# Kernel tuning notes

Measured on AMD Instinct MI355X. Metric: run time of the kernel, lower is better.

Reference implementation:

```python
import jax, jax.numpy as jnp
import numpy as np

N = 200000          # num nodes (num_rus)
E = 12800000        # num edges (avg degree 64)
IN_C, HID, OUT = 1, 16, 4


def setup_inputs() -> dict:
    key = jax.random.key(0)
    ks = jax.random.split(key, 6)
    x = jax.random.normal(ks[0], (N, IN_C), dtype=jnp.float32)
    edges = jax.random.randint(ks[1], (2, E), 0, N, dtype=jnp.int64)
    W1 = jax.random.normal(ks[2], (IN_C, HID), dtype=jnp.float32) / np.sqrt(IN_C)
    b1 = jnp.zeros((HID,), dtype=jnp.float32)
    W2 = jax.random.normal(ks[3], (HID, HID), dtype=jnp.float32) / np.sqrt(HID)
    b2 = jnp.zeros((HID,), dtype=jnp.float32)
    Wl = jax.random.normal(ks[4], (HID, OUT), dtype=jnp.float32) / np.sqrt(HID)
    bl = jnp.zeros((OUT,), dtype=jnp.float32)
    return {"x": x, "edges": edges, "W1": W1, "b1": b1, "W2": W2, "b2": b2, "Wl": Wl, "bl": bl}


def _gcn_norm(edges):
    # PyG GCNConv default: add self-loops, symmetric normalization.
    loops = jnp.arange(N, dtype=edges.dtype)
    src = jnp.concatenate([edges[0], loops])   # [E+N]
    dst = jnp.concatenate([edges[1], loops])
    deg = jax.ops.segment_sum(jnp.ones_like(dst, dtype=jnp.float32), dst, num_segments=N)
    dinv = jnp.where(deg > 0, jax.lax.rsqrt(deg), 0.0)
    norm = dinv[src] * dinv[dst]               # [E+N]
    return src, dst, norm


def _gcn_conv(h, W, b, src, dst, norm):
    m = h @ W                                  # [N, out] transform first (cheap, small C)
    msgs = m[src] * norm[:, None]              # gather + normalize, [E+N, out]
    agg = jax.ops.segment_sum(msgs, dst, num_segments=N)
    return agg + b


def reference(x, edges, W1, b1, W2, b2, Wl, bl):
    src, dst, norm = _gcn_norm(edges)
    h = jax.nn.relu(_gcn_conv(x, W1, b1, src, dst, norm))
    h = jax.nn.relu(_gcn_conv(h, W2, b2, src, dst, norm))
    return h @ Wl + bl                         # [N, 4]
```

## Files before the change

kernel.cpp:

```cpp
#include <hip/hip_runtime.h>

#define HID 16
#define OUTC 4
#define G 64
#define SBSH 8
#define SBN 256
#define CAP 21504
#define PHSH 16
#define SUBK 8
#define KB (SBN * SUBK)
#define PBLK 512
#define NPB_MAX 800
#define NPB_H 400
#define STCAP 46
#define STP 47
#define EPB 16
#define EPP (PBLK * EPB)
#define SENT 0xFFFFFFFFu

__device__ __forceinline__ float relu(float v) { return v > 0.f ? v : 0.f; }

__global__ void k_cnt(const int* __restrict__ dst, int* __restrict__ cnt,
                      int E, int nsb, int nc, int ncsh) {
    __shared__ int lc[NPB_MAX];
    for (int i = threadIdx.x; i < nsb; i += PBLK) lc[i] = 0;
    __syncthreads();
    int c = blockIdx.x;
    int chunk = (E + nc - 1) / nc;
    int lo = c * chunk, hi = lo + chunk < E ? lo + chunk : E;
    for (int i = lo + threadIdx.x; i < hi; i += PBLK * 4) {
#pragma unroll
        for (int u = 0; u < 4; ++u) {
            int ii = i + u * PBLK;
            if (ii < hi) atomicAdd(lc + (dst[ii] >> SBSH), 1);
        }
    }
    __syncthreads();
    for (int b = threadIdx.x; b < nsb; b += PBLK)
        cnt[(b << ncsh) + c] = (lc[b] + 15) & ~15;
}

__global__ void k_scanA(int* __restrict__ a, int* __restrict__ bsum, int L) {
    __shared__ int s[1024];
    int i = blockIdx.x * 1024 + threadIdx.x;
    int v = (i < L) ? a[i] : 0;
    s[threadIdx.x] = v; __syncthreads();
    for (int off = 1; off < 1024; off <<= 1) {
        int t = (threadIdx.x >= (unsigned)off) ? s[threadIdx.x - off] : 0;
        __syncthreads();
        s[threadIdx.x] += t;
        __syncthreads();
    }
    if (i < L) a[i] = s[threadIdx.x] - v;
    if (threadIdx.x == 1023) bsum[blockIdx.x] = s[1023];
}

__global__ void k_scanB(int* __restrict__ bsum, int SB) {
    __shared__ int s[1024];
    int carry = 0;
    for (int base = 0; base < SB; base += 1024) {
        int idx = base + threadIdx.x;
        int v = (idx < SB) ? bsum[idx] : 0;
        s[threadIdx.x] = v; __syncthreads();
        for (int off = 1; off < 1024; off <<= 1) {
            int t = (threadIdx.x >= (unsigned)off) ? s[threadIdx.x - off] : 0;
            __syncthreads();
            s[threadIdx.x] += t;
            __syncthreads();
        }
        if (idx < SB) bsum[idx] = carry + s[threadIdx.x] - v;
        carry += s[1023];
        __syncthreads();
    }
    if (threadIdx.x == 0) bsum[SB] = carry;
}

__global__ void k_scanC(int* __restrict__ a, const int* __restrict__ bsum,
                        int* __restrict__ bOff, int L, int nsb, int SB,
                        int nc, int ncsh) {
    int i = blockIdx.x * 1024 + threadIdx.x;
    if (i < L) {
        int v = a[i] + bsum[blockIdx.x];
        a[i] = v;
        if ((i & (nc - 1)) == 0) bOff[i >> ncsh] = v;
    }
    if (blockIdx.x == 0 && threadIdx.x == 0) bOff[nsb] = bsum[SB];
}

__global__ void __launch_bounds__(PBLK) k_part(const int* __restrict__ src,
                                               const int* __restrict__ dst,
                                               const int* __restrict__ cnt,
                                               unsigned int* __restrict__ rec,
                                               int E, int nsb, int nc, int ncsh) {
    __shared__ unsigned int stage[NPB_H * STP];
    __shared__ int scnt[NPB_H];
    __shared__ int gcur[NPB_H];
    int c = blockIdx.x >> 1, h = blockIdx.x & 1;
    int nh = (nsb - h + 1) >> 1;
    for (int bh = threadIdx.x; bh < nh; bh += PBLK) {
        scnt[bh] = 0;
        gcur[bh] = cnt[((bh * 2 + h) << ncsh) + c];
    }
    __syncthreads();
    int chunk = (E + nc - 1) / nc;
    int lo = c * chunk, hi = lo + chunk < E ? lo + chunk : E;
    int g4 = threadIdx.x >> 2, r4 = threadIdx.x & 3;
    for (int base = lo; base < hi; base += EPP) {
#pragma unroll 4
        for (int k = 0; k < EPB; ++k) {
            int i = base + k * PBLK + threadIdx.x;
            if (i < hi) {
                int d = dst[i], s = src[i];
                int b = d >> SBSH;
                if ((b & 1) == h) {
                    int bh = b >> 1;
                    int pos = atomicAdd(scnt + bh, 1);
                    if (pos < STCAP)
                        stage[bh * STP + pos] = (unsigned int)s | ((unsigned int)(d & (SBN - 1)) << 18);
                }
            }
        }
        __syncthreads();
        for (int bh = g4; bh < nh; bh += PBLK / 4) {
            int n = scnt[bh];
            int f = n & ~15;
            if (f > 0) {
                int gc = gcur[bh];
                for (int j = 0; j < f; j += 16) {
                    const unsigned int* sp = &stage[bh * STP + j] + r4 * 4;
                    ((uint4*)&rec[gc + j])[r4] = make_uint4(sp[0], sp[1], sp[2], sp[3]);
                }
                if (r4 == 0) {
                    gcur[bh] = gc + f;
                    for (int jj = 0; jj < n - f; ++jj)
                        stage[bh * STP + jj] = stage[bh * STP + f + jj];
                    scnt[bh] = n - f;
                }
            }
        }
        __syncthreads();
    }
    for (int bh = threadIdx.x; bh < nh; bh += PBLK) {
        int n = scnt[bh];
        if (n > 0) {
            unsigned int tmp[16];
            for (int j = 0; j < 16; ++j) tmp[j] = (j < n) ? stage[bh * STP + j] : SENT;
            uint4* d4 = (uint4*)&rec[gcur[bh]];
            d4[0] = make_uint4(tmp[0], tmp[1], tmp[2], tmp[3]);
            d4[1] = make_uint4(tmp[4], tmp[5], tmp[6], tmp[7]);
            d4[2] = make_uint4(tmp[8], tmp[9], tmp[10], tmp[11]);
            d4[3] = make_uint4(tmp[12], tmp[13], tmp[14], tmp[15]);
        }
    }
}

__global__ void __launch_bounds__(256) k_sort(const int* __restrict__ bOff,
                                              unsigned int* __restrict__ rec,
                                              float* __restrict__ dinv,
                                              int* __restrict__ rowp,
                                              int N, int nsb, int E) {
    __shared__ unsigned int raw[CAP];
    __shared__ int hist[KB], cur[KB];
    __shared__ int s[256];
    int b = blockIdx.x;
    int beg = bOff[b], end = bOff[b + 1];
    int size = end - beg; if (size > CAP) size = CAP;
    {
        uint4* raw4 = (uint4*)raw;
        const uint4* rec4 = (const uint4*)&rec[beg];
        int size4 = size >> 2;
        for (int i = threadIdx.x; i < size4; i += 256) raw4[i] = rec4[i];
    }
    for (int k = threadIdx.x; k < KB; k += 256) hist[k] = 0;
    __syncthreads();
    for (int i = threadIdx.x; i < size; i += 1024) {
#pragma unroll
        for (int u = 0; u < 4; ++u) {
            int ii = i + u * 256;
            if (ii < size) {
                unsigned int r = raw[ii];
                if (r != SENT) {
                    int key = (int)((r >> 18) << 3) | (int)((r & 0x3FFFF) >> PHSH);
                    atomicAdd(hist + key, 1);
                }
            }
        }
    }
    __syncthreads();
    int t = threadIdx.x;
    int psum = 0;
#pragma unroll
    for (int j = 0; j < SUBK; ++j) psum += hist[t * SUBK + j];
    s[t] = psum; __syncthreads();
    for (int off = 1; off < 256; off <<= 1) {
        int v = (t >= off) ? s[t - off] : 0;
        __syncthreads();
        s[t] += v;
        __syncthreads();
    }
    int ex = s[t] - psum;
    {
        int n = b * SBN + t;
        bool valid = (n < N);
        int running = ex;
#pragma unroll
        for (int j = 0; j < SUBK; ++j) {
            cur[t * SUBK + j] = running;
            if (valid) rowp[(size_t)n * SUBK + j] = beg + running;
            running += hist[t * SUBK + j];
        }
        if (valid) dinv[n] = rsqrtf((float)psum + 1.0f);
    }
    __syncthreads();
    for (int i = t; i < size; i += 1024) {
#pragma unroll
        for (int u = 0; u < 4; ++u) {
            int ii = i + u * 256;
            if (ii < size) {
                unsigned int r = raw[ii];
                if (r != SENT) {
                    int key = (int)((r >> 18) << 3) | (int)((r & 0x3FFFF) >> PHSH);
                    int p = atomicAdd(cur + key, 1);
                    rec[beg + p] = r & 0x3FFFF;
                }
            }
        }
    }
}

__global__ void k_m1(const float* __restrict__ x, const float* __restrict__ W1,
                     const float* __restrict__ dinv, float* __restrict__ m, int N) {
    int t = blockIdx.x * blockDim.x + threadIdx.x;
    if (t < N * HID) {
        int n = t >> 4, c = t & 15;
        m[t] = x[n] * W1[c] * dinv[n];
    }
}

__global__ void k_m2(float4* __restrict__ h4, const float* __restrict__ W2,
                     const float* __restrict__ dinv, int N) {
    __shared__ float hs[64][HID + 1];
    __shared__ float w[HID * HID];
    if (threadIdx.x < HID * HID) w[threadIdx.x] = W2[threadIdx.x];
    int idx = blockIdx.x * 256 + threadIdx.x;
    int n = idx >> 2, q = idx & 3;
    int ln = threadIdx.x >> 2;
    if (n < N) {
        float4 v = h4[idx];
        hs[ln][q * 4 + 0] = v.x; hs[ln][q * 4 + 1] = v.y;
        hs[ln][q * 4 + 2] = v.z; hs[ln][q * 4 + 3] = v.w;
    }
    __syncthreads();
    if (n < N) {
        float dn = dinv[n];
        float4 acc = make_float4(0.f, 0.f, 0.f, 0.f);
        const float* hr = hs[ln];
#pragma unroll
        for (int ci = 0; ci < HID; ++ci) {
            float hv = hr[ci];
            const float* wr = w + ci * HID + q * 4;
            acc.x += hv * wr[0]; acc.y += hv * wr[1];
            acc.z += hv * wr[2]; acc.w += hv * wr[3];
        }
        acc.x *= dn; acc.y *= dn; acc.z *= dn; acc.w *= dn;
        h4[idx] = acc;
    }
}

template <int MODE>
__global__ void __launch_bounds__(256) k_aggp(const int* __restrict__ rowp,
                                              const unsigned int* __restrict__ adj,
                                              const float* __restrict__ dinv,
                                              const float4* __restrict__ mS4,
                                              float4* __restrict__ gagg4,
                                              const float4* __restrict__ b4,
                                              const float* __restrict__ Wl,
                                              const float* __restrict__ bl,
                                              float* __restrict__ out,
                                              int N, int p) {
    __shared__ float hs[G][HID + 1];
    __shared__ float wl[HID * OUTC];
    __shared__ float blv[OUTC];
    if (MODE == 2) {
        if (threadIdx.x < HID * OUTC) wl[threadIdx.x] = Wl[threadIdx.x];
        if (threadIdx.x < OUTC) blv[threadIdx.x] = bl[threadIdx.x];
    }
    int dl = threadIdx.x >> 2, q = threadIdx.x & 3;
    int n = blockIdx.x * G + dl;
    if (n < N) {
        int i = rowp[(size_t)n * SUBK + p];
        int end = rowp[(size_t)n * SUBK + p + 1];
        float4 acc = (p == 0) ? mS4[n * 4 + q] : gagg4[n * 4 + q];
        for (; i + 8 <= end; i += 8) {
            int s0 = adj[i] * 4 + q, s1 = adj[i + 1] * 4 + q;
            int s2 = adj[i + 2] * 4 + q, s3 = adj[i + 3] * 4 + q;
            int s4 = adj[i + 4] * 4 + q, s5 = adj[i + 5] * 4 + q;
            int s6 = adj[i + 6] * 4 + q, s7 = adj[i + 7] * 4 + q;
            float4 v0 = mS4[s0], v1 = mS4[s1], v2 = mS4[s2], v3 = mS4[s3];
            float4 v4 = mS4[s4], v5 = mS4[s5], v6 = mS4[s6], v7 = mS4[s7];
            acc.x += (v0.x + v1.x + v2.x + v3.x) + (v4.x + v5.x + v6.x + v7.x);
            acc.y += (v0.y + v1.y + v2.y + v3.y) + (v4.y + v5.y + v6.y + v7.y);
            acc.z += (v0.z + v1.z + v2.z + v3.z) + (v4.z + v5.z + v6.z + v7.z);
            acc.w += (v0.w + v1.w + v2.w + v3.w) + (v4.w + v5.w + v6.w + v7.w);
        }
        for (; i + 4 <= end; i += 4) {
            int s0 = adj[i] * 4 + q, s1 = adj[i + 1] * 4 + q;
            int s2 = adj[i + 2] * 4 + q, s3 = adj[i + 3] * 4 + q;
            float4 v0 = mS4[s0], v1 = mS4[s1], v2 = mS4[s2], v3 = mS4[s3];
            acc.x += v0.x + v1.x + v2.x + v3.x;
            acc.y += v0.y + v1.y + v2.y + v3.y;
            acc.z += v0.z + v1.z + v2.z + v3.z;
            acc.w += v0.w + v1.w + v2.w + v3.w;
        }
        for (; i < end; ++i) {
            float4 v = mS4[adj[i] * 4 + q];
            acc.x += v.x; acc.y += v.y; acc.z += v.z; acc.w += v.w;
        }
        if (MODE == 0) {
            gagg4[n * 4 + q] = acc;
        } else {
            float dn = dinv[n];
            float4 bb = b4[q];
            float4 h;
            h.x = relu(acc.x * dn + bb.x);
            h.y = relu(acc.y * dn + bb.y);
            h.z = relu(acc.z * dn + bb.z);
            h.w = relu(acc.w * dn + bb.w);
            if (MODE == 1) {
                gagg4[n * 4 + q] = h;
            } else {
                hs[dl][q * 4 + 0] = h.x; hs[dl][q * 4 + 1] = h.y;
                hs[dl][q * 4 + 2] = h.z; hs[dl][q * 4 + 3] = h.w;
            }
        }
    }
    if (MODE == 2) {
        __syncthreads();
        if (n < N) {
            float acc = blv[q];
            const float* hr = hs[dl];
#pragma unroll
            for (int ci = 0; ci < HID; ++ci) acc += hr[ci] * wl[ci * OUTC + q];
            out[n * OUTC + q] = acc;
        }
    }
}

static inline size_t alignup(size_t v, size_t a) { return (v + a - 1) & ~(a - 1); }

extern "C" void kernel_launch(void* const* d_in, const int* in_sizes, int n_in,
                              void* d_out, int out_size, void* d_ws, size_t ws_size,
                              hipStream_t stream) {
    const float* x  = (const float*)d_in[0];
    const int* ed   = (const int*)d_in[1];
    const float* W1 = (const float*)d_in[2];
    const float* b1 = (const float*)d_in[3];
    const float* W2 = (const float*)d_in[4];
    const float* b2 = (const float*)d_in[5];
    const float* Wl = (const float*)d_in[6];
    const float* bl = (const float*)d_in[7];
    float* out      = (float*)d_out;

    int N = in_sizes[0];
    int E = in_sizes[1] / 2;
    const int* src = ed;
    const int* dst = ed + E;
    int nsb = (N + SBN - 1) / SBN;
    int nb64 = (N + G - 1) / G;
    int nphase = (N + (1 << PHSH) - 1) >> PHSH;

    int nc = 256, ncsh = 8;
    size_t o = 0;
    float* dinv; int* rowp; int* bsum; int* bOff; unsigned int* rec;
    float* bufA; float* bufB;
    char* w = (char*)d_ws;
    for (int attempt = 0; attempt < 2; ++attempt) {
        int L = nsb * nc;
        int SB = (L + 1023) / 1024;
        size_t Epad = (size_t)E + 15 * (size_t)L;
        o = 0;
        dinv = (float*)(w + o); o = alignup(o + (size_t)N * 4, 64);
        rowp = (int*)(w + o);   o = alignup(o + (size_t)N * SUBK * 4, 64);
        bsum = (int*)(w + o);   o = alignup(o + ((size_t)SB + 1) * 4, 64);
        bOff = (int*)(w + o);   o = alignup(o + ((size_t)nsb + 1) * 4, 64);
        rec  = (unsigned int*)(w + o); o = alignup(o + Epad * 4, 64);
        bufA = (float*)(w + o); o = alignup(o + (size_t)N * HID * 4, 64);
        bufB = (float*)(w + o); o = alignup(o + (size_t)N * HID * 4, 64);
        if (o <= ws_size || nc == 128) break;
        nc = 128; ncsh = 7;
    }
    int L = nsb * nc;
    int SB = (L + 1023) / 1024;
    int* cnt = (int*)bufA;

    int blk = 256;
    int gN16 = (N * HID + blk - 1) / blk;

    k_cnt<<<nc, PBLK, 0, stream>>>(dst, cnt, E, nsb, nc, ncsh);
    k_scanA<<<SB, 1024, 0, stream>>>(cnt, bsum, L);
    k_scanB<<<1, 1024, 0, stream>>>(bsum, SB);
    k_scanC<<<SB, 1024, 0, stream>>>(cnt, bsum, bOff, L, nsb, SB, nc, ncsh);
    k_part<<<nc * 2, PBLK, 0, stream>>>(src, dst, cnt, rec, E, nsb, nc, ncsh);
    k_sort<<<nsb, 256, 0, stream>>>(bOff, rec, dinv, rowp, N, nsb, E);

    k_m1<<<gN16, blk, 0, stream>>>(x, W1, dinv, bufA, N);
    for (int p = 0; p < nphase; ++p) {
        if (p < nphase - 1)
            k_aggp<0><<<nb64, blk, 0, stream>>>(rowp, rec, dinv, (const float4*)bufA,
                                                (float4*)bufB, (const float4*)b1,
                                                nullptr, nullptr, nullptr, N, p);
        else
            k_aggp<1><<<nb64, blk, 0, stream>>>(rowp, rec, dinv, (const float4*)bufA,
                                                (float4*)bufB, (const float4*)b1,
                                                nullptr, nullptr, nullptr, N, p);
    }

    k_m2<<<nb64, blk, 0, stream>>>((float4*)bufB, W2, dinv, N);
    for (int p = 0; p < nphase; ++p) {
        if (p < nphase - 1)
            k_aggp<0><<<nb64, blk, 0, stream>>>(rowp, rec, dinv, (const float4*)bufB,
                                                (float4*)bufA, (const float4*)b2,
                                                nullptr, nullptr, nullptr, N, p);
        else
            k_aggp<2><<<nb64, blk, 0, stream>>>(rowp, rec, dinv, (const float4*)bufB,
                                                (float4*)bufA, (const float4*)b2,
                                                Wl, bl, out, N, p);
    }
}
```

Baseline: 538.2 us.

## Partition all superbuckets in one k_part block per chunk instead of two halves

k_part used to launch two blocks per edge chunk, each staging only the even or the odd superbuckets, so every edge's src/dst was read twice. Now one block per chunk stages all superbuckets in a single larger shared-memory buffer (784 buckets × 45 slots), so edge input is read only once. In exchange each block needs far more LDS (about 147KB), which likely limits each CU to one resident block. There are also half as many blocks and a slightly smaller per-bucket staging capacity, which reduces parallelism and latency hiding in this pass.

```diff
diff --git a/kernel.cpp b/kernel.cpp
--- a/kernel.cpp
+++ b/kernel.cpp
@@ -10,10 +10,9 @@
 #define SUBK 8
 #define KB (SBN * SUBK)
 #define PBLK 512
-#define NPB_MAX 800
-#define NPB_H 400
-#define STCAP 46
-#define STP 47
+#define NPB_MAX 784
+#define STCAP 45
+#define STP 45
 #define EPB 16
 #define EPP (PBLK * EPB)
 #define SENT 0xFFFFFFFFu
@@ -92,14 +91,13 @@
                                                const int* __restrict__ cnt,
                                                unsigned int* __restrict__ rec,
                                                int E, int nsb, int nc, int ncsh) {
-    __shared__ unsigned int stage[NPB_H * STP];
-    __shared__ int scnt[NPB_H];
-    __shared__ int gcur[NPB_H];
-    int c = blockIdx.x >> 1, h = blockIdx.x & 1;
-    int nh = (nsb - h + 1) >> 1;
-    for (int bh = threadIdx.x; bh < nh; bh += PBLK) {
-        scnt[bh] = 0;
-        gcur[bh] = cnt[((bh * 2 + h) << ncsh) + c];
+    __shared__ unsigned int stage[NPB_MAX * STP];
+    __shared__ int scnt[NPB_MAX];
+    __shared__ int gcur[NPB_MAX];
+    int c = blockIdx.x;
+    for (int b = threadIdx.x; b < nsb; b += PBLK) {
+        scnt[b] = 0;
+        gcur[b] = cnt[(b << ncsh) + c];
     }
     __syncthreads();
     int chunk = (E + nc - 1) / nc;
@@ -112,40 +110,37 @@
             if (i < hi) {
                 int d = dst[i], s = src[i];
                 int b = d >> SBSH;
-                if ((b & 1) == h) {
-                    int bh = b >> 1;
-                    int pos = atomicAdd(scnt + bh, 1);
-                    if (pos < STCAP)
-                        stage[bh * STP + pos] = (unsigned int)s | ((unsigned int)(d & (SBN - 1)) << 18);
-                }
+                int pos = atomicAdd(scnt + b, 1);
+                if (pos < STCAP)
+                    stage[b * STP + pos] = (unsigned int)s | ((unsigned int)(d & (SBN - 1)) << 18);
             }
         }
         __syncthreads();
-        for (int bh = g4; bh < nh; bh += PBLK / 4) {
-            int n = scnt[bh];
+        for (int b = g4; b < nsb; b += PBLK / 4) {
+            int n = scnt[b];
             int f = n & ~15;
             if (f > 0) {
-                int gc = gcur[bh];
+                int gc = gcur[b];
                 for (int j = 0; j < f; j += 16) {
-                    const unsigned int* sp = &stage[bh * STP + j] + r4 * 4;
+                    const unsigned int* sp = &stage[b * STP + j] + r4 * 4;
                     ((uint4*)&rec[gc + j])[r4] = make_uint4(sp[0], sp[1], sp[2], sp[3]);
                 }
                 if (r4 == 0) {
-                    gcur[bh] = gc + f;
+                    gcur[b] = gc + f;
                     for (int jj = 0; jj < n - f; ++jj)
-                        stage[bh * STP + jj] = stage[bh * STP + f + jj];
-                    scnt[bh] = n - f;
+                        stage[b * STP + jj] = stage[b * STP + f + jj];
+                    scnt[b] = n - f;
                 }
             }
         }
         __syncthreads();
     }
-    for (int bh = threadIdx.x; bh < nh; bh += PBLK) {
-        int n = scnt[bh];
+    for (int b = threadIdx.x; b < nsb; b += PBLK) {
+        int n = scnt[b];
         if (n > 0) {
             unsigned int tmp[16];
-            for (int j = 0; j < 16; ++j) tmp[j] = (j < n) ? stage[bh * STP + j] : SENT;
-            uint4* d4 = (uint4*)&rec[gcur[bh]];
+            for (int j = 0; j < 16; ++j) tmp[j] = (j < n) ? stage[b * STP + j] : SENT;
+            uint4* d4 = (uint4*)&rec[gcur[b]];
             d4[0] = make_uint4(tmp[0], tmp[1], tmp[2], tmp[3]);
             d4[1] = make_uint4(tmp[4], tmp[5], tmp[6], tmp[7]);
             d4[2] = make_uint4(tmp[8], tmp[9], tmp[10], tmp[11]);
@@ -400,7 +395,7 @@
     k_scanA<<<SB, 1024, 0, stream>>>(cnt, bsum, L);
     k_scanB<<<1, 1024, 0, stream>>>(bsum, SB);
     k_scanC<<<SB, 1024, 0, stream>>>(cnt, bsum, bOff, L, nsb, SB, nc, ncsh);
-    k_part<<<nc * 2, PBLK, 0, stream>>>(src, dst, cnt, rec, E, nsb, nc, ncsh);
+    k_part<<<nc, PBLK, 0, stream>>>(src, dst, cnt, rec, E, nsb, nc, ncsh);
     k_sort<<<nsb, 256, 0, stream>>>(bOff, rec, dinv, rowp, N, nsb, E);
 
     k_m1<<<gN16, blk, 0, stream>>>(x, W1, dinv, bufA, N);
```

New measurement: 543.4 us. Within noise of the previous version (+1.0%).

## Fuse both GCN layers into one cooperative kernel with grid syncs

Applied to the files above, without the earlier changes.

Replaces the per-phase sequence of k_m1, k_aggp and k_m2 launches with a single cooperative kernel. Each thread owns one node, keeps its 16-wide accumulator in registers across the phases, and uses grid.sync between phases instead of kernel boundaries. This removes launch overhead and the intermediate writes and reads of the aggregation buffers. In exchange it runs only N/1024 blocks of 1024 threads (about 196), which may leave the GPU underused for the gather-heavy work, and one thread per node can see load imbalance. The old launch path remains as a fallback if the cooperative launch fails.

```diff
diff --git a/kernel.cpp b/kernel.cpp
--- a/kernel.cpp
+++ b/kernel.cpp
@@ -1,4 +1,5 @@
 #include <hip/hip_runtime.h>
+#include <hip/hip_cooperative_groups.h>
 
 #define HID 16
 #define OUTC 4
@@ -18,6 +19,8 @@
 #define EPP (PBLK * EPB)
 #define SENT 0xFFFFFFFFu
 
+namespace cg = cooperative_groups;
+
 __device__ __forceinline__ float relu(float v) { return v > 0.f ? v : 0.f; }
 
 __global__ void k_cnt(const int* __restrict__ dst, int* __restrict__ cnt,
@@ -225,6 +228,142 @@
                 }
             }
         }
+    }
+}
+
+__global__ void __launch_bounds__(1024, 4)
+k_net(const int* __restrict__ rowp, const unsigned int* __restrict__ adj,
+      const float* __restrict__ dinv, const float* __restrict__ x,
+      const float* __restrict__ W1, const float* __restrict__ b1,
+      const float* __restrict__ W2, const float* __restrict__ b2,
+      const float* __restrict__ Wl, const float* __restrict__ bl,
+      float4* __restrict__ mS1, float4* __restrict__ mS2,
+      float4* __restrict__ out4, int N, int nphase) {
+    cg::grid_group grid = cg::this_grid();
+    __shared__ float w1s[HID], b1s[HID], b2s[HID], bls[OUTC];
+    __shared__ float w2s[HID * HID];
+    __shared__ float wls[HID * OUTC];
+    if (threadIdx.x < HID * HID) w2s[threadIdx.x] = W2[threadIdx.x];
+    if (threadIdx.x < HID * OUTC) wls[threadIdx.x] = Wl[threadIdx.x];
+    if (threadIdx.x < HID) {
+        w1s[threadIdx.x] = W1[threadIdx.x];
+        b1s[threadIdx.x] = b1[threadIdx.x];
+        b2s[threadIdx.x] = b2[threadIdx.x];
+    }
+    if (threadIdx.x < OUTC) bls[threadIdx.x] = bl[threadIdx.x];
+    __syncthreads();
+
+    int n = blockIdx.x * 1024 + threadIdx.x;
+    bool valid = (n < N);
+    float dn = valid ? dinv[n] : 0.f;
+    float acc[HID];
+
+    if (valid) {
+        float xv = x[n];
+#pragma unroll
+        for (int c = 0; c < HID; ++c) acc[c] = xv * w1s[c] * dn;
+        float4* d4 = &mS1[(size_t)n * 4];
+        d4[0] = make_float4(acc[0], acc[1], acc[2], acc[3]);
+        d4[1] = make_float4(acc[4], acc[5], acc[6], acc[7]);
+        d4[2] = make_float4(acc[8], acc[9], acc[10], acc[11]);
+        d4[3] = make_float4(acc[12], acc[13], acc[14], acc[15]);
+    }
+    grid.sync();
+
+    for (int p = 0; p < nphase; ++p) {
+        if (valid) {
+            int i = rowp[(size_t)n * SUBK + p];
+            int end = rowp[(size_t)n * SUBK + p + 1];
+            for (; i + 2 <= end; i += 2) {
+                const float4* A = &mS1[(size_t)adj[i] * 4];
+                const float4* B = &mS1[(size_t)adj[i + 1] * 4];
+                float4 a0 = A[0], a1 = A[1], a2 = A[2], a3 = A[3];
+                float4 c0 = B[0], c1 = B[1], c2 = B[2], c3 = B[3];
+                acc[0] += a0.x + c0.x;  acc[1] += a0.y + c0.y;
+                acc[2] += a0.z + c0.z;  acc[3] += a0.w + c0.w;
+                acc[4] += a1.x + c1.x;  acc[5] += a1.y + c1.y;
+                acc[6] += a1.z + c1.z;  acc[7] += a1.w + c1.w;
+                acc[8] += a2.x + c2.x;  acc[9] += a2.y + c2.y;
+                acc[10] += a2.z + c2.z; acc[11] += a2.w + c2.w;
+                acc[12] += a3.x + c3.x; acc[13] += a3.y + c3.y;
+                acc[14] += a3.z + c3.z; acc[15] += a3.w + c3.w;
+            }
+            for (; i < end; ++i) {
+                const float4* A = &mS1[(size_t)adj[i] * 4];
+                float4 a0 = A[0], a1 = A[1], a2 = A[2], a3 = A[3];
+                acc[0] += a0.x;  acc[1] += a0.y;  acc[2] += a0.z;  acc[3] += a0.w;
+                acc[4] += a1.x;  acc[5] += a1.y;  acc[6] += a1.z;  acc[7] += a1.w;
+                acc[8] += a2.x;  acc[9] += a2.y;  acc[10] += a2.z; acc[11] += a2.w;
+                acc[12] += a3.x; acc[13] += a3.y; acc[14] += a3.z; acc[15] += a3.w;
+            }
+        }
+        if (p < nphase - 1) grid.sync();
+    }
+
+    float h[HID];
+#pragma unroll
+    for (int c = 0; c < HID; ++c) h[c] = relu(acc[c] * dn + b1s[c]);
+    float m2[HID];
+#pragma unroll
+    for (int co = 0; co < HID; ++co) {
+        float sum = 0.f;
+#pragma unroll
+        for (int ci = 0; ci < HID; ++ci) sum += h[ci] * w2s[ci * HID + co];
+        m2[co] = sum * dn;
+    }
+    if (valid) {
+        float4* d4 = &mS2[(size_t)n * 4];
+        d4[0] = make_float4(m2[0], m2[1], m2[2], m2[3]);
+        d4[1] = make_float4(m2[4], m2[5], m2[6], m2[7]);
+        d4[2] = make_float4(m2[8], m2[9], m2[10], m2[11]);
+        d4[3] = make_float4(m2[12], m2[13], m2[14], m2[15]);
+    }
+    grid.sync();
+
+#pragma unroll
+    for (int c = 0; c < HID; ++c) acc[c] = m2[c];
+    for (int p = 0; p < nphase; ++p) {
+        if (valid) {
+            int i = rowp[(size_t)n * SUBK + p];
+            int end = rowp[(size_t)n * SUBK + p + 1];
+            for (; i + 2 <= end; i += 2) {
+                const float4* A = &mS2[(size_t)adj[i] * 4];
+                const float4* B = &mS2[(size_t)adj[i + 1] * 4];
+                float4 a0 = A[0], a1 = A[1], a2 = A[2], a3 = A[3];
+                float4 c0 = B[0], c1 = B[1], c2 = B[2], c3 = B[3];
+                acc[0] += a0.x + c0.x;  acc[1] += a0.y + c0.y;
+                acc[2] += a0.z + c0.z;  acc[3] += a0.w + c0.w;
+                acc[4] += a1.x + c1.x;  acc[5] += a1.y + c1.y;
+                acc[6] += a1.z + c1.z;  acc[7] += a1.w + c1.w;
+                acc[8] += a2.x + c2.x;  acc[9] += a2.y + c2.y;
+                acc[10] += a2.z + c2.z; acc[11] += a2.w + c2.w;
+                acc[12] += a3.x + c3.x; acc[13] += a3.y + c3.y;
+                acc[14] += a3.z + c3.z; acc[15] += a3.w + c3.w;
+            }
+            for (; i < end; ++i) {
+                const float4* A = &mS2[(size_t)adj[i] * 4];
+                float4 a0 = A[0], a1 = A[1], a2 = A[2], a3 = A[3];
+                acc[0] += a0.x;  acc[1] += a0.y;  acc[2] += a0.z;  acc[3] += a0.w;
+                acc[4] += a1.x;  acc[5] += a1.y;  acc[6] += a1.z;  acc[7] += a1.w;
+                acc[8] += a2.x;  acc[9] += a2.y;  acc[10] += a2.z; acc[11] += a2.w;
+                acc[12] += a3.x; acc[13] += a3.y; acc[14] += a3.z; acc[15] += a3.w;
+            }
+        }
+        if (p < nphase - 1) grid.sync();
+    }
+
+    if (valid) {
+#pragma unroll
+        for (int c = 0; c < HID; ++c) h[c] = relu(acc[c] * dn + b2s[c]);
+        float o[OUTC];
+#pragma unroll
+        for (int co = 0; co < OUTC; ++co) {
+            float sum = bls[co];
+#pragma unroll
+            for (int ci = 0; ci < HID; ++ci) sum += h[ci] * wls[ci * OUTC + co];
+            o[co] = sum;
+        }
+        out4[n] = make_float4(o[0], o[1], o[2], o[3]);
     }
 }
 
@@ -403,27 +542,46 @@
     k_part<<<nc * 2, PBLK, 0, stream>>>(src, dst, cnt, rec, E, nsb, nc, ncsh);
     k_sort<<<nsb, 256, 0, stream>>>(bOff, rec, dinv, rowp, N, nsb, E);
 
-    k_m1<<<gN16, blk, 0, stream>>>(x, W1, dinv, bufA, N);
-    for (int p = 0; p < nphase; ++p) {
-        if (p < nphase - 1)
-            k_aggp<0><<<nb64, blk, 0, stream>>>(rowp, rec, dinv, (const float4*)bufA,
-                                                (float4*)bufB, (const float4*)b1,
-                                                nullptr, nullptr, nullptr, N, p);
-        else
-            k_aggp<1><<<nb64, blk, 0, stream>>>(rowp, rec, dinv, (const float4*)bufA,
-                                                (float4*)bufB, (const float4*)b1,
-                                                nullptr, nullptr, nullptr, N, p);
-    }
-
-    k_m2<<<nb64, blk, 0, stream>>>((float4*)bufB, W2, dinv, N);
-    for (int p = 0; p < nphase; ++p) {
-        if (p < nphase - 1)
-            k_aggp<0><<<nb64, blk, 0, stream>>>(rowp, rec, dinv, (const float4*)bufB,
-                                                (float4*)bufA, (const float4*)b2,
-                                                nullptr, nullptr, nullptr, N, p);
-        else
-            k_aggp<2><<<nb64, blk, 0, stream>>>(rowp, rec, dinv, (const float4*)bufB,
-                                                (float4*)bufA, (const float4*)b2,
-                                                Wl, bl, out, N, p);
-    }
-}
+    int nblk = (N + 1023) >> 10;
+    bool coop_ok = false;
+    if (nblk <= 256) {
+        float4* mS1 = (float4*)bufA;
+        float4* mS2 = (float4*)bufB;
+        float4* out4 = (float4*)out;
+        void* args[] = {
+            (void*)&rowp, (void*)&rec, (void*)&dinv, (void*)&x,
+            (void*)&W1, (void*)&b1, (void*)&W2, (void*)&b2,
+            (void*)&Wl, (void*)&bl,
+            (void*)&mS1, (void*)&mS2, (void*)&out4,
+            (void*)&N, (void*)&nphase
+        };
+        hipError_t err = hipLaunchCooperativeKernel((const void*)k_net, dim3(nblk),
+                                                    dim3(1024), args, 0, stream);
+        coop_ok = (err == hipSuccess);
+    }
+
+    if (!coop_ok) {
+        k_m1<<<gN16, blk, 0, stream>>>(x, W1, dinv, bufA, N);
+        for (int p = 0; p < nphase; ++p) {
+            if (p < nphase - 1)
+                k_aggp<0><<<nb64, blk, 0, stream>>>(rowp, rec, dinv, (const float4*)bufA,
+                                                    (float4*)bufB, (const float4*)b1,
+                                                    nullptr, nullptr, nullptr, N, p);
+            else
+                k_aggp<1><<<nb64, blk, 0, stream>>>(rowp, rec, dinv, (const float4*)bufA,
+                                                    (float4*)bufB, (const float4*)b1,
+                                                    nullptr, nullptr, nullptr, N, p);
+        }
+        k_m2<<<nb64, blk, 0, stream>>>((float4*)bufB, W2, dinv, N);
+        for (int p = 0; p < nphase; ++p) {
+            if (p < nphase - 1)
+                k_aggp<0><<<nb64, blk, 0, stream>>>(rowp, rec, dinv, (const float4*)bufB,
+                                                    (float4*)bufA, (const float4*)b2,
+                                                    nullptr, nullptr, nullptr, N, p);
+            else
+                k_aggp<2><<<nb64, blk, 0, stream>>>(rowp, rec, dinv, (const float4*)bufB,
+                                                    (float4*)bufA, (const float4*)b2,
+                                                    Wl, bl, out, N, p);
+        }
+    }
+}
```

Result: slower. 939.2 us (+74.5%).
